# Kernel optimization log

Measured on AMD Instinct MI355X. Metric: run time of the kernel, lower is better.

The kernel has to match this reference:

```python
import jax, jax.numpy as jnp
import numpy as np

NB_HEAD = 16
DIM_PER_HEAD = 64
EMB = 1024
B, SQ, SK = 4, 2048, 2048


def setup_inputs() -> dict:
    key = jax.random.key(0)
    ks = jax.random.split(key, 8)
    scale = 1.0 / np.sqrt(EMB)
    return {
        "hidden_state_query": jax.random.normal(ks[0], (B, SQ, EMB), jnp.float32),
        "hidden_state_key": jax.random.normal(ks[1], (B, SK, EMB), jnp.float32),
        "hidden_state_value": jax.random.normal(ks[2], (B, SK, EMB), jnp.float32),
        "attention_mask": jax.random.randint(ks[3], (B, SQ, SK), 0, 2).astype(bool),
        "Wq": jax.random.uniform(ks[4], (NB_HEAD * DIM_PER_HEAD, EMB), jnp.float32, -scale, scale),
        "Wk": jax.random.uniform(ks[5], (NB_HEAD * DIM_PER_HEAD, EMB), jnp.float32, -scale, scale),
        "Wv": jax.random.uniform(ks[6], (NB_HEAD * DIM_PER_HEAD, EMB), jnp.float32, -scale, scale),
        "Wo": jax.random.uniform(ks[7], (EMB, NB_HEAD * DIM_PER_HEAD), jnp.float32, -scale, scale),
    }


def reference(hidden_state_query, hidden_state_key, hidden_state_value,
              attention_mask, Wq, Wk, Wv, Wo):
    bs, sq, _ = hidden_state_query.shape
    sk = hidden_state_key.shape[1]
    # projections (nn.Linear without bias: x @ W.T)
    q = (hidden_state_query @ Wq.T).reshape(bs, sq, NB_HEAD, DIM_PER_HEAD).transpose(0, 2, 1, 3)
    k = (hidden_state_key @ Wk.T).reshape(bs, sk, NB_HEAD, DIM_PER_HEAD).transpose(0, 2, 1, 3)
    v = (hidden_state_value @ Wv.T).reshape(bs, sk, NB_HEAD, DIM_PER_HEAD).transpose(0, 2, 1, 3)
    scores = jnp.einsum('bhqd,bhkd->bhqk', q, k) / jnp.sqrt(jnp.asarray(DIM_PER_HEAD, q.dtype))
    attn = jax.nn.softmax(scores, axis=-1)
    # POST-softmax zero masking (True -> 0), broadcast over heads; no renormalization
    attn = jnp.where(attention_mask[:, None, :, :], jnp.asarray(0.0, attn.dtype), attn)
    ctx = jnp.einsum('bhqk,bhkd->bhqd', attn, v)  # [B,H,Sq,Dh]
    ctx = ctx.transpose(0, 2, 1, 3).reshape(bs, sq, NB_HEAD * DIM_PER_HEAD)
    return ctx @ Wo.T + hidden_state_query
```

## Files before the change

kernel.cpp:

```cpp
#include <hip/hip_runtime.h>
#include <hip/hip_bf16.h>
#include <stdint.h>

typedef __bf16 bf16_t;
typedef bf16_t bf16x2 __attribute__((ext_vector_type(2)));
typedef bf16_t bf16x8 __attribute__((ext_vector_type(8)));
typedef float  f32x4  __attribute__((ext_vector_type(4)));
typedef float  f32x16 __attribute__((ext_vector_type(16)));
typedef unsigned uint2v __attribute__((ext_vector_type(2)));

#define NB_HEAD 16
#define DH      64
#define EMB     1024
#define BATCH   4
#define SEQ     2048
#define NTOK    (BATCH*SEQ)

#define QSCALE 0.1803368801111204f

__device__ __forceinline__ void gload_lds16(const void* g, void* l) {
  __builtin_amdgcn_global_load_lds(
      (const __attribute__((address_space(1))) void*)g,
      (__attribute__((address_space(3))) void*)l, 16, 0, 0);
}

__device__ __forceinline__ uint32_t pkbf(float a, float b) {
  bf16x2 v = { (bf16_t)a, (bf16_t)b };
  return __builtin_bit_cast(uint32_t, v);
}

__device__ __forceinline__ void cvt8_body(const float* __restrict__ in,
                                          bf16_t* __restrict__ out, int i) {
  const float4* p = reinterpret_cast<const float4*>(in) + (size_t)i * 2;
  float4 a = p[0], b = p[1];
  uint4 r;
  r.x = pkbf(a.x, a.y); r.y = pkbf(a.z, a.w);
  r.z = pkbf(b.x, b.y); r.w = pkbf(b.z, b.w);
  reinterpret_cast<uint4*>(out)[i] = r;
}

__device__ __forceinline__ void mkand_body(const uint8_t* __restrict__ m,
                                           uint16_t* __restrict__ out, int i) {
  uint2 v = reinterpret_cast<const uint2*>(m)[i];
  uint4 r;
  uint32_t lo = v.x, hi = v.y;
  uint16_t e[8];
#pragma unroll
  for (int j = 0; j < 4; j++) e[j]     = (uint16_t)(((lo >> (8 * j)) & 0xFF) - 1);
#pragma unroll
  for (int j = 0; j < 4; j++) e[4 + j] = (uint16_t)(((hi >> (8 * j)) & 0xFF) - 1);
  r.x = (uint32_t)e[0] | ((uint32_t)e[1] << 16);
  r.y = (uint32_t)e[2] | ((uint32_t)e[3] << 16);
  r.z = (uint32_t)e[4] | ((uint32_t)e[5] << 16);
  r.w = (uint32_t)e[6] | ((uint32_t)e[7] << 16);
  reinterpret_cast<uint4*>(out)[i] = r;
}

__global__ void __launch_bounds__(256)
prep(const float* __restrict__ hq, const float* __restrict__ hk,
     const float* __restrict__ hv, const float* __restrict__ Wq,
     const float* __restrict__ Wk, const float* __restrict__ Wv,
     const float* __restrict__ Wo,
     bf16_t* hq_b, bf16_t* hk_b, bf16_t* hv_b,
     bf16_t* Wq_b, bf16_t* Wk_b, bf16_t* Wv_b, bf16_t* Wo_b,
     const uint8_t* __restrict__ mask, uint16_t* __restrict__ mand) {
  const int bid = blockIdx.x;
  if (bid < 12288) {
    const int seg = bid >> 12;
    const float* src = seg == 0 ? hq : seg == 1 ? hk : hv;
    bf16_t*      dst = seg == 0 ? hq_b : seg == 1 ? hk_b : hv_b;
    cvt8_body(src, dst, (bid & 4095) * 256 + (int)threadIdx.x);
  } else if (bid < 14336) {
    const int sb = bid - 12288;
    const int seg = sb >> 9;
    const float* src = seg == 0 ? Wq : seg == 1 ? Wk : seg == 2 ? Wv : Wo;
    bf16_t*      dst = seg == 0 ? Wq_b : seg == 1 ? Wk_b : seg == 2 ? Wv_b : Wo_b;
    cvt8_body(src, dst, (sb & 511) * 256 + (int)threadIdx.x);
  } else {
    mkand_body(mask, mand, (bid - 14336) * 256 + (int)threadIdx.x);
  }
}

__global__ void __launch_bounds__(256)
mkand(const uint8_t* __restrict__ m, uint16_t* __restrict__ out) {
  mkand_body(m, out, blockIdx.x * 256 + (int)threadIdx.x);
}

#define BM 128
#define BN 128
#define BKT 32

__global__ void __launch_bounds__(256, 4)
gemm_qkv3(const bf16_t* __restrict__ hq_b, const bf16_t* __restrict__ hk_b,
          const bf16_t* __restrict__ hv_b,
          const bf16_t* __restrict__ Wq_b, const bf16_t* __restrict__ Wk_b,
          const bf16_t* __restrict__ Wv_b,
          bf16_t* __restrict__ Qb, bf16_t* __restrict__ Kf,
          bf16_t* __restrict__ Vf) {
  __shared__ bf16_t As[2][BM * BKT];
  __shared__ bf16_t Bs[2][BN * BKT];
  const int K = EMB, N = EMB;
  const int z = blockIdx.z;
  const bf16_t* A  = z == 0 ? hq_b : z == 1 ? hk_b : hv_b;
  const bf16_t* Bw = z == 0 ? Wq_b : z == 1 ? Wk_b : Wv_b;

  const int t    = threadIdx.x;
  const int lane = t & 63, w = t >> 6;
  const int wr = w >> 1, wc = w & 1;
  const int l15 = lane & 15, l4 = lane >> 4;

  const int lin = blockIdx.x + 8 * blockIdx.y;
  const int nl  = (lin & 7) * 64 + (lin >> 3);
  const int rowBase = (nl >> 3) * BM, colBase = (nl & 7) * BN;

  f32x4 acc[4][4];
#pragma unroll
  for (int i = 0; i < 4; i++)
#pragma unroll
    for (int j = 0; j < 4; j++) acc[i][j] = f32x4{0.f, 0.f, 0.f, 0.f};

  const int t16 = t * 16;

#pragma unroll
  for (int i = 0; i < 2; ++i) {
    int off  = i * 4096 + t16;
    int row  = off >> 6, colb = off & 63;
    gload_lds16((const char*)A  + (((size_t)(rowBase + row)) * K) * 2 + colb, (char*)As[0] + off);
    gload_lds16((const char*)Bw + (((size_t)(colBase + row)) * K) * 2 + colb, (char*)Bs[0] + off);
  }
  __syncthreads();

  int cur = 0;
  for (int k0 = 0; k0 < K; k0 += BKT) {
    if (k0 + BKT < K) {
      const int nb = cur ^ 1;
#pragma unroll
      for (int i = 0; i < 2; ++i) {
        int off  = i * 4096 + t16;
        int row  = off >> 6, colb = off & 63;
        gload_lds16((const char*)A  + (((size_t)(rowBase + row)) * K + k0 + BKT) * 2 + colb, (char*)As[nb] + off);
        gload_lds16((const char*)Bw + (((size_t)(colBase + row)) * K + k0 + BKT) * 2 + colb, (char*)Bs[nb] + off);
      }
    }
    {
      bf16x8 af[4], bfb[4];
#pragma unroll
      for (int mi = 0; mi < 4; mi++)
        af[mi] = *reinterpret_cast<const bf16x8*>(
            &As[cur][(wr * 64 + mi * 16 + l15) * BKT + l4 * 8]);
#pragma unroll
      for (int ni = 0; ni < 4; ni++)
        bfb[ni] = *reinterpret_cast<const bf16x8*>(
            &Bs[cur][(wc * 64 + ni * 16 + l15) * BKT + l4 * 8]);
      __builtin_amdgcn_s_setprio(1);
#pragma unroll
      for (int mi = 0; mi < 4; mi++)
#pragma unroll
        for (int ni = 0; ni < 4; ni++)
          acc[mi][ni] = __builtin_amdgcn_mfma_f32_16x16x32_bf16(
              af[mi], bfb[ni], acc[mi][ni], 0, 0, 0);
      __builtin_amdgcn_s_setprio(0);
    }
    __syncthreads();
    cur ^= 1;
  }

#pragma unroll
  for (int mi = 0; mi < 4; mi++) {
#pragma unroll
    for (int ni = 0; ni < 4; ni++) {
      const int m0 = rowBase + wr * 64 + mi * 16 + l4 * 4;
      const int n  = colBase + wc * 64 + ni * 16 + l15;
      if (z == 0) {
#pragma unroll
        for (int r = 0; r < 4; r++)
          Qb[(size_t)(m0 + r) * EMB + n] = (bf16_t)(acc[mi][ni][r] * QSCALE);
      } else if (z == 1) {
#pragma unroll
        for (int r = 0; r < 4; r++) {
          int m = m0 + r;
          const int bq = m >> 11, s = m & 2047, hh = n >> 6, d = n & 63;
          size_t local = (size_t)(s >> 6) * 4096 + ((s >> 5) & 1) * 2048 +
                         (d >> 4) * 512 + ((d >> 3) & 1) * 256 + (s & 31) * 8 + (d & 7);
          Kf[(size_t)(bq * 16 + hh) * 131072 + local] = (bf16_t)acc[mi][ni][r];
        }
      } else {
        const int bq = m0 >> 11, s0 = m0 & 2047, hh = n >> 6, d = n & 63;
        size_t local = (size_t)(s0 >> 6) * 4096 + ((s0 >> 4) & 3) * 1024 +
                       (d >> 5) * 512 + ((s0 >> 3) & 1) * 256 + (d & 31) * 8 + (s0 & 7);
        uint2 st;
        st.x = pkbf(acc[mi][ni][0], acc[mi][ni][1]);
        st.y = pkbf(acc[mi][ni][2], acc[mi][ni][3]);
        *reinterpret_cast<uint2*>(Vf + (size_t)(bq * 16 + hh) * 131072 + local) = st;
      }
    }
  }
}

__global__ void __launch_bounds__(256, 4)
gemm_out(const bf16_t* __restrict__ A, const bf16_t* __restrict__ Bw,
         float* __restrict__ Cf, const float* __restrict__ resid) {
  __shared__ bf16_t As[2][BM * BKT];
  __shared__ bf16_t Bs[2][BN * BKT];
  const int K = EMB, N = EMB;
  const int t    = threadIdx.x;
  const int lane = t & 63, w = t >> 6;
  const int wr = w >> 1, wc = w & 1;
  const int l15 = lane & 15, l4 = lane >> 4;

  const int lin = blockIdx.x + 8 * blockIdx.y;
  const int nl  = (lin & 7) * 64 + (lin >> 3);
  const int rowBase = (nl >> 3) * BM, colBase = (nl & 7) * BN;

  f32x4 acc[4][4];
#pragma unroll
  for (int i = 0; i < 4; i++)
#pragma unroll
    for (int j = 0; j < 4; j++) acc[i][j] = f32x4{0.f, 0.f, 0.f, 0.f};

  const int t16 = t * 16;

#pragma unroll
  for (int i = 0; i < 2; ++i) {
    int off  = i * 4096 + t16;
    int row  = off >> 6, colb = off & 63;
    gload_lds16((const char*)A  + (((size_t)(rowBase + row)) * K) * 2 + colb, (char*)As[0] + off);
    gload_lds16((const char*)Bw + (((size_t)(colBase + row)) * K) * 2 + colb, (char*)Bs[0] + off);
  }
  __syncthreads();

  int cur = 0;
  for (int k0 = 0; k0 < K; k0 += BKT) {
    if (k0 + BKT < K) {
      const int nb = cur ^ 1;
#pragma unroll
      for (int i = 0; i < 2; ++i) {
        int off  = i * 4096 + t16;
        int row  = off >> 6, colb = off & 63;
        gload_lds16((const char*)A  + (((size_t)(rowBase + row)) * K + k0 + BKT) * 2 + colb, (char*)As[nb] + off);
        gload_lds16((const char*)Bw + (((size_t)(colBase + row)) * K + k0 + BKT) * 2 + colb, (char*)Bs[nb] + off);
      }
    }
    {
      bf16x8 af[4], bfb[4];
#pragma unroll
      for (int mi = 0; mi < 4; mi++)
        af[mi] = *reinterpret_cast<const bf16x8*>(
            &As[cur][(wr * 64 + mi * 16 + l15) * BKT + l4 * 8]);
#pragma unroll
      for (int ni = 0; ni < 4; ni++)
        bfb[ni] = *reinterpret_cast<const bf16x8*>(
            &Bs[cur][(wc * 64 + ni * 16 + l15) * BKT + l4 * 8]);
      __builtin_amdgcn_s_setprio(1);
#pragma unroll
      for (int mi = 0; mi < 4; mi++)
#pragma unroll
        for (int ni = 0; ni < 4; ni++)
          acc[mi][ni] = __builtin_amdgcn_mfma_f32_16x16x32_bf16(
              af[mi], bfb[ni], acc[mi][ni], 0, 0, 0);
      __builtin_amdgcn_s_setprio(0);
    }
    __syncthreads();
    cur ^= 1;
  }

#pragma unroll
  for (int mi = 0; mi < 4; mi++) {
#pragma unroll
    for (int ni = 0; ni < 4; ni++) {
      const int m0 = rowBase + wr * 64 + mi * 16 + l4 * 4;
      const int n  = colBase + wc * 64 + ni * 16 + l15;
#pragma unroll
      for (int r = 0; r < 4; r++) {
        int m = m0 + r;
        Cf[(size_t)m * N + n] = acc[mi][ni][r] + resid[(size_t)m * N + n];
      }
    }
  }
}

__global__ void __launch_bounds__(512, 2)
attn32(const bf16_t* __restrict__ Qb, const bf16_t* __restrict__ Kh,
       const bf16_t* __restrict__ Vt, const uint16_t* __restrict__ Mand,
       bf16_t* __restrict__ ctx) {
  __shared__ __align__(16) bf16_t Ks[2][64 * 64];
  __shared__ __align__(16) bf16_t Vs[2][64 * 64];

  const int t = threadIdx.x, lane = t & 63, wid = t >> 6;
  const int q = lane & 31, hi = lane >> 5;
  const int l16 = lane * 16;

  const int lin = blockIdx.x + 8 * (blockIdx.y + 16 * blockIdx.z);
  const int nl  = (lin & 7) * 64 + (lin >> 3);
  const int bx = nl & 7, h = (nl >> 3) & 15, b = nl >> 7;

  const int q0 = bx * 256 + wid * 32;
  const int qrow = b * SEQ + q0 + q;

  const char* kg = (const char*)(Kh + ((size_t)(b * NB_HEAD + h)) * SEQ * DH);
  const char* vg = (const char*)(Vt + ((size_t)(b * NB_HEAD + h)) * SEQ * DH);

  const bf16_t* qp = Qb + (size_t)qrow * EMB + h * DH + hi * 8;
  bf16x8 qf[4];
#pragma unroll
  for (int d = 0; d < 4; d++) qf[d] = *reinterpret_cast<const bf16x8*>(qp + d * 16);

  f32x16 o0 = {0}, o1 = {0};
  float lrun = 0.f;
  const uint16_t* mbase = Mand + (size_t)qrow * SEQ;

  gload_lds16(kg + t * 16, (char*)Ks[0] + t * 16);
  gload_lds16(vg + t * 16, (char*)Vs[0] + t * 16);
  __syncthreads();

  int cur = 0;
  for (int kb = 0; kb < SEQ; kb += 64) {
    if (kb + 64 < SEQ) {
      const int nb = cur ^ 1;
      gload_lds16(kg + (size_t)(kb + 64) * 128 + t * 16, (char*)Ks[nb] + t * 16);
      gload_lds16(vg + (size_t)(kb + 64) * 128 + t * 16, (char*)Vs[nb] + t * 16);
    }

    const char* kls = (const char*)Ks[cur];
    f32x16 p0 = {0}, p1 = {0};
    __builtin_amdgcn_s_setprio(1);
#pragma unroll
    for (int dsl = 0; dsl < 4; dsl++) {
      bf16x8 kf0 = *reinterpret_cast<const bf16x8*>(kls + dsl * 1024 + l16);
      bf16x8 kf1 = *reinterpret_cast<const bf16x8*>(kls + 4096 + dsl * 1024 + l16);
      p0 = __builtin_amdgcn_mfma_f32_32x32x16_bf16(kf0, qf[dsl], p0, 0, 0, 0);
      p1 = __builtin_amdgcn_mfma_f32_32x32x16_bf16(kf1, qf[dsl], p1, 0, 0, 0);
    }
    __builtin_amdgcn_s_setprio(0);

    uint4 mv[4];
#pragma unroll
    for (int ks = 0; ks < 4; ks++)
      mv[ks] = *reinterpret_cast<const uint4*>(mbase + kb + 16 * ks + 8 * hi);

    float ps = 0.f;
#pragma unroll
    for (int i = 0; i < 16; i++) { p0[i] = __builtin_amdgcn_exp2f(p0[i]); ps += p0[i]; }
#pragma unroll
    for (int i = 0; i < 16; i++) { p1[i] = __builtin_amdgcn_exp2f(p1[i]); ps += p1[i]; }
    ps += __shfl_xor(ps, 32);
    lrun += ps;

    const char* vls = (const char*)Vs[cur];
#pragma unroll
    for (int ks = 0; ks < 4; ks++) {
      const int s8 = (ks & 1) * 8;
      float e0, e1, e2, e3, e4, e5, e6, e7;
      if (ks < 2) {
        e0 = p0[s8+0]; e1 = p0[s8+1]; e2 = p0[s8+2]; e3 = p0[s8+3];
        e4 = p0[s8+4]; e5 = p0[s8+5]; e6 = p0[s8+6]; e7 = p0[s8+7];
      } else {
        e0 = p1[s8+0]; e1 = p1[s8+1]; e2 = p1[s8+2]; e3 = p1[s8+3];
        e4 = p1[s8+4]; e5 = p1[s8+5]; e6 = p1[s8+6]; e7 = p1[s8+7];
      }
      uint32_t a0 = pkbf(e0, e1), a1 = pkbf(e2, e3);
      uint32_t a2 = pkbf(e4, e5), a3 = pkbf(e6, e7);
      uint2v s02 = __builtin_amdgcn_permlane32_swap(a0, a2, false, false);
      uint2v s13 = __builtin_amdgcn_permlane32_swap(a1, a3, false, false);
      uint4 fr;
      fr.x = s02[0]; fr.y = s13[0]; fr.z = s02[1]; fr.w = s13[1];
      fr.x &= mv[ks].x; fr.y &= mv[ks].y; fr.z &= mv[ks].z; fr.w &= mv[ks].w;
      bf16x8 pa = __builtin_bit_cast(bf16x8, fr);
      bf16x8 vf0 = *reinterpret_cast<const bf16x8*>(vls + ks * 2048 + l16);
      bf16x8 vf1 = *reinterpret_cast<const bf16x8*>(vls + ks * 2048 + 1024 + l16);
      __builtin_amdgcn_s_setprio(1);
      o0 = __builtin_amdgcn_mfma_f32_32x32x16_bf16(vf0, pa, o0, 0, 0, 0);
      o1 = __builtin_amdgcn_mfma_f32_32x32x16_bf16(vf1, pa, o1, 0, 0, 0);
      __builtin_amdgcn_s_setprio(0);
    }

    __syncthreads();
    cur ^= 1;
  }

  float inv = 1.0f / lrun;
  bf16_t* cp = ctx + (size_t)qrow * EMB + h * DH;
#pragma unroll
  for (int g = 0; g < 4; g++) {
    uint2 st;
    st.x = pkbf(o0[4*g+0] * inv, o0[4*g+1] * inv);
    st.y = pkbf(o0[4*g+2] * inv, o0[4*g+3] * inv);
    *reinterpret_cast<uint2*>(cp + 8 * g + 4 * hi) = st;
    st.x = pkbf(o1[4*g+0] * inv, o1[4*g+1] * inv);
    st.y = pkbf(o1[4*g+2] * inv, o1[4*g+3] * inv);
    *reinterpret_cast<uint2*>(cp + 32 + 8 * g + 4 * hi) = st;
  }
}

extern "C" void kernel_launch(void* const* d_in, const int* in_sizes, int n_in,
                              void* d_out, int out_size, void* d_ws, size_t ws_size,
                              hipStream_t stream) {
  const float*   hq   = (const float*)d_in[0];
  const float*   hk   = (const float*)d_in[1];
  const float*   hv   = (const float*)d_in[2];
  const uint8_t* mask = (const uint8_t*)d_in[3];
  const float*   Wq   = (const float*)d_in[4];
  const float*   Wk   = (const float*)d_in[5];
  const float*   Wv   = (const float*)d_in[6];
  const float*   Wo   = (const float*)d_in[7];
  float* out = (float*)d_out;

  char* ws = (char*)d_ws;
  const size_t SZ_H = (size_t)NTOK * EMB * 2;
  const size_t SZ_W = (size_t)EMB * EMB * 2;
  bf16_t* hq_b = (bf16_t*)(ws + 0 * SZ_H);
  bf16_t* hk_b = (bf16_t*)(ws + 1 * SZ_H);
  bf16_t* hv_b = (bf16_t*)(ws + 2 * SZ_H);
  bf16_t* Qb   = (bf16_t*)(ws + 3 * SZ_H);
  bf16_t* Kf   = (bf16_t*)(ws + 4 * SZ_H);
  bf16_t* Vf   = (bf16_t*)(ws + 5 * SZ_H);
  bf16_t* ctx  = (bf16_t*)(ws + 6 * SZ_H);
  bf16_t* Wq_b = (bf16_t*)(ws + 7 * SZ_H + 0 * SZ_W);
  bf16_t* Wk_b = (bf16_t*)(ws + 7 * SZ_H + 1 * SZ_W);
  bf16_t* Wv_b = (bf16_t*)(ws + 7 * SZ_H + 2 * SZ_W);
  bf16_t* Wo_b = (bf16_t*)(ws + 7 * SZ_H + 3 * SZ_W);

  const size_t MAND_OFF = 7 * SZ_H + 4 * SZ_W;
  const size_t MAND_SZ  = (size_t)BATCH * SEQ * SEQ * 2;
  const bool bigws = ws_size >= MAND_OFF + MAND_SZ;
  uint16_t* Mand = bigws ? (uint16_t*)(ws + MAND_OFF) : (uint16_t*)ws;

  prep<<<bigws ? 22528 : 14336, 256, 0, stream>>>(
      hq, hk, hv, Wq, Wk, Wv, Wo,
      hq_b, hk_b, hv_b, Wq_b, Wk_b, Wv_b, Wo_b, mask, Mand);

  gemm_qkv3<<<dim3(8, 64, 3), 256, 0, stream>>>(hq_b, hk_b, hv_b,
                                                Wq_b, Wk_b, Wv_b, Qb, Kf, Vf);

  if (!bigws) mkand<<<8192, 256, 0, stream>>>(mask, Mand);

  attn32<<<dim3(SEQ / 256, NB_HEAD, BATCH), 512, 0, stream>>>(Qb, Kf, Vf, Mand, ctx);

  gemm_out<<<dim3(8, 64), 256, 0, stream>>>(ctx, Wo_b, out, hq);
}
```

Baseline: 229.7 us.

## Split attention key range in two halves and reduce partial outputs

The attention kernel becomes a template. When the large workspace is available, each block handles half of the key sequence, which doubles the grid. Each half writes unnormalized fp32 partial outputs and row sums, into the output buffer and a reused workspace region. A new reduce kernel then adds the halves, normalizes and writes bf16 ctx. The aim is more parallel blocks per query tile, paid for with extra fp32 global traffic and one more kernel launch.

```diff
diff --git a/kernel.cpp b/kernel.cpp
--- a/kernel.cpp
+++ b/kernel.cpp
@@ -99,7 +99,7 @@
           bf16_t* __restrict__ Vf) {
   __shared__ bf16_t As[2][BM * BKT];
   __shared__ bf16_t Bs[2][BN * BKT];
-  const int K = EMB, N = EMB;
+  const int K = EMB;
   const int z = blockIdx.z;
   const bf16_t* A  = z == 0 ? hq_b : z == 1 ? hk_b : hv_b;
   const bf16_t* Bw = z == 0 ? Wq_b : z == 1 ? Wk_b : Wv_b;
@@ -279,10 +279,12 @@
   }
 }
 
+template<int SPLIT>
 __global__ void __launch_bounds__(512, 2)
 attn32(const bf16_t* __restrict__ Qb, const bf16_t* __restrict__ Kh,
        const bf16_t* __restrict__ Vt, const uint16_t* __restrict__ Mand,
-       bf16_t* __restrict__ ctx) {
+       bf16_t* __restrict__ ctx, float* __restrict__ O0, float* __restrict__ O1,
+       float* __restrict__ L0, float* __restrict__ L1) {
   __shared__ __align__(16) bf16_t Ks[2][64 * 64];
   __shared__ __align__(16) bf16_t Vs[2][64 * 64];
 
@@ -290,15 +292,20 @@
   const int q = lane & 31, hi = lane >> 5;
   const int l16 = lane * 16;
 
-  const int lin = blockIdx.x + 8 * (blockIdx.y + 16 * blockIdx.z);
-  const int nl  = (lin & 7) * 64 + (lin >> 3);
-  const int bx = nl & 7, h = (nl >> 3) & 15, b = nl >> 7;
+  const int lin = blockIdx.x + (SPLIT ? 16 : 8) * (blockIdx.y + 16 * blockIdx.z);
+  const int nl  = (lin & 7) * (SPLIT ? 128 : 64) + (lin >> 3);
+  int half, bx, h, b;
+  if (SPLIT) { half = nl & 1; bx = (nl >> 1) & 7; h = (nl >> 4) & 15; b = nl >> 8; }
+  else       { half = 0;      bx = nl & 7;        h = (nl >> 3) & 15; b = nl >> 7; }
 
   const int q0 = bx * 256 + wid * 32;
   const int qrow = b * SEQ + q0 + q;
-
-  const char* kg = (const char*)(Kh + ((size_t)(b * NB_HEAD + h)) * SEQ * DH);
-  const char* vg = (const char*)(Vt + ((size_t)(b * NB_HEAD + h)) * SEQ * DH);
+  const int NT = SPLIT ? 16 : 32;
+
+  const char* kg = (const char*)(Kh + ((size_t)(b * NB_HEAD + h)) * SEQ * DH)
+                   + (size_t)half * 16 * 8192;
+  const char* vg = (const char*)(Vt + ((size_t)(b * NB_HEAD + h)) * SEQ * DH)
+                   + (size_t)half * 16 * 8192;
 
   const bf16_t* qp = Qb + (size_t)qrow * EMB + h * DH + hi * 8;
   bf16x8 qf[4];
@@ -307,18 +314,18 @@
 
   f32x16 o0 = {0}, o1 = {0};
   float lrun = 0.f;
-  const uint16_t* mbase = Mand + (size_t)qrow * SEQ;
+  const uint16_t* mbase = Mand + (size_t)qrow * SEQ + half * (SEQ / 2) * SPLIT;
 
   gload_lds16(kg + t * 16, (char*)Ks[0] + t * 16);
   gload_lds16(vg + t * 16, (char*)Vs[0] + t * 16);
   __syncthreads();
 
   int cur = 0;
-  for (int kb = 0; kb < SEQ; kb += 64) {
-    if (kb + 64 < SEQ) {
+  for (int tt = 0; tt < NT; ++tt) {
+    if (tt + 1 < NT) {
       const int nb = cur ^ 1;
-      gload_lds16(kg + (size_t)(kb + 64) * 128 + t * 16, (char*)Ks[nb] + t * 16);
-      gload_lds16(vg + (size_t)(kb + 64) * 128 + t * 16, (char*)Vs[nb] + t * 16);
+      gload_lds16(kg + (size_t)(tt + 1) * 8192 + t * 16, (char*)Ks[nb] + t * 16);
+      gload_lds16(vg + (size_t)(tt + 1) * 8192 + t * 16, (char*)Vs[nb] + t * 16);
     }
 
     const char* kls = (const char*)Ks[cur];
@@ -336,7 +343,7 @@
     uint4 mv[4];
 #pragma unroll
     for (int ks = 0; ks < 4; ks++)
-      mv[ks] = *reinterpret_cast<const uint4*>(mbase + kb + 16 * ks + 8 * hi);
+      mv[ks] = *reinterpret_cast<const uint4*>(mbase + tt * 64 + 16 * ks + 8 * hi);
 
     float ps = 0.f;
 #pragma unroll
@@ -378,18 +385,50 @@
     cur ^= 1;
   }
 
-  float inv = 1.0f / lrun;
-  bf16_t* cp = ctx + (size_t)qrow * EMB + h * DH;
-#pragma unroll
-  for (int g = 0; g < 4; g++) {
-    uint2 st;
-    st.x = pkbf(o0[4*g+0] * inv, o0[4*g+1] * inv);
-    st.y = pkbf(o0[4*g+2] * inv, o0[4*g+3] * inv);
-    *reinterpret_cast<uint2*>(cp + 8 * g + 4 * hi) = st;
-    st.x = pkbf(o1[4*g+0] * inv, o1[4*g+1] * inv);
-    st.y = pkbf(o1[4*g+2] * inv, o1[4*g+3] * inv);
-    *reinterpret_cast<uint2*>(cp + 32 + 8 * g + 4 * hi) = st;
-  }
+  if (SPLIT) {
+    float* op = (half ? O1 : O0) + (size_t)qrow * EMB + h * DH;
+#pragma unroll
+    for (int g = 0; g < 4; g++) {
+      float4 s0 = { o0[4*g+0], o0[4*g+1], o0[4*g+2], o0[4*g+3] };
+      float4 s1 = { o1[4*g+0], o1[4*g+1], o1[4*g+2], o1[4*g+3] };
+      *reinterpret_cast<float4*>(op + 8 * g + 4 * hi) = s0;
+      *reinterpret_cast<float4*>(op + 32 + 8 * g + 4 * hi) = s1;
+    }
+    if (hi == 0) (half ? L1 : L0)[qrow * NB_HEAD + h] = lrun;
+  } else {
+    float inv = 1.0f / lrun;
+    bf16_t* cp = ctx + (size_t)qrow * EMB + h * DH;
+#pragma unroll
+    for (int g = 0; g < 4; g++) {
+      uint2 st;
+      st.x = pkbf(o0[4*g+0] * inv, o0[4*g+1] * inv);
+      st.y = pkbf(o0[4*g+2] * inv, o0[4*g+3] * inv);
+      *reinterpret_cast<uint2*>(cp + 8 * g + 4 * hi) = st;
+      st.x = pkbf(o1[4*g+0] * inv, o1[4*g+1] * inv);
+      st.y = pkbf(o1[4*g+2] * inv, o1[4*g+3] * inv);
+      *reinterpret_cast<uint2*>(cp + 32 + 8 * g + 4 * hi) = st;
+    }
+  }
+}
+
+__global__ void __launch_bounds__(256)
+reduce_ctx(const float* __restrict__ O0, const float* __restrict__ O1,
+           const float* __restrict__ L0, const float* __restrict__ L1,
+           bf16_t* __restrict__ ctx) {
+  const int i = blockIdx.x * 256 + (int)threadIdx.x;
+  const size_t base = (size_t)i * 8;
+  const int qh = (int)(base >> 6);
+  const float inv = 1.0f / (L0[qh] + L1[qh]);
+  float4 a0 = *reinterpret_cast<const float4*>(O0 + base);
+  float4 a1 = *reinterpret_cast<const float4*>(O0 + base + 4);
+  float4 b0 = *reinterpret_cast<const float4*>(O1 + base);
+  float4 b1 = *reinterpret_cast<const float4*>(O1 + base + 4);
+  uint4 r;
+  r.x = pkbf((a0.x + b0.x) * inv, (a0.y + b0.y) * inv);
+  r.y = pkbf((a0.z + b0.z) * inv, (a0.w + b0.w) * inv);
+  r.z = pkbf((a1.x + b1.x) * inv, (a1.y + b1.y) * inv);
+  r.w = pkbf((a1.z + b1.z) * inv, (a1.w + b1.w) * inv);
+  reinterpret_cast<uint4*>(ctx)[i] = r;
 }
 
 extern "C" void kernel_launch(void* const* d_in, const int* in_sizes, int n_in,
@@ -425,6 +464,11 @@
   const bool bigws = ws_size >= MAND_OFF + MAND_SZ;
   uint16_t* Mand = bigws ? (uint16_t*)(ws + MAND_OFF) : (uint16_t*)ws;
 
+  float* O0 = (float*)d_out;
+  float* O1 = (float*)(ws + 0);
+  float* L0 = (float*)(ws + 2 * SZ_H);
+  float* L1 = (float*)(ws + 2 * SZ_H + 512 * 1024);
+
   prep<<<bigws ? 22528 : 14336, 256, 0, stream>>>(
       hq, hk, hv, Wq, Wk, Wv, Wo,
       hq_b, hk_b, hv_b, Wq_b, Wk_b, Wv_b, Wo_b, mask, Mand);
@@ -434,7 +478,14 @@
 
   if (!bigws) mkand<<<8192, 256, 0, stream>>>(mask, Mand);
 
-  attn32<<<dim3(SEQ / 256, NB_HEAD, BATCH), 512, 0, stream>>>(Qb, Kf, Vf, Mand, ctx);
+  if (bigws) {
+    attn32<1><<<dim3(16, NB_HEAD, BATCH), 512, 0, stream>>>(
+        Qb, Kf, Vf, Mand, nullptr, O0, O1, L0, L1);
+    reduce_ctx<<<NTOK * EMB / 8 / 256, 256, 0, stream>>>(O0, O1, L0, L1, ctx);
+  } else {
+    attn32<0><<<dim3(8, NB_HEAD, BATCH), 512, 0, stream>>>(
+        Qb, Kf, Vf, Mand, ctx, nullptr, nullptr, nullptr, nullptr);
+  }
 
   gemm_out<<<dim3(8, 64), 256, 0, stream>>>(ctx, Wo_b, out, hq);
 }
```

Result: slower. 256.0 us (+11.4%).
